# Performance work log

Measured on AMD Instinct MI355X. Metric: run time of the kernel, lower is better.

Reference implementation:

```python
import jax, jax.numpy as jnp
import numpy as np

B, L, R, D = 4, 1024, 4, 1024   # batch, seq, expansion rate, model dim
HEADS, HD, FF = 16, 64, 4096
EPS = 1e-6


def _static_alpha(layer_id):
    a0 = np.zeros((R, 1), np.float32)
    a0[layer_id % R, 0] = 1.0
    return jnp.asarray(np.concatenate([a0, np.eye(R, dtype=np.float32)], axis=1))  # [R, R+1]


def setup_inputs() -> dict:
    key = jax.random.key(0)
    ks = jax.random.split(key, 12)
    w = lambda k, shape, s=0.02: (jax.random.normal(k, shape, jnp.float32) * s)
    return {
        "H": jax.random.normal(ks[0], (B, L, R, D), jnp.float32),
        # attention hyper-connection (layer_id*2 = 0)
        "hc1_norm_w": jnp.ones((D,), jnp.float32),
        "hc1_alpha_fn": w(ks[1], (D, R + 1), 0.01),
        "hc1_beta_fn": w(ks[2], (D,), 0.01),
        "hc1_a_scale": jnp.full((1,), 0.01, jnp.float32),
        "hc1_b_scale": jnp.full((1,), 0.01, jnp.float32),
        "hc1_s_alpha": _static_alpha(0),
        "hc1_s_beta": jnp.ones((R,), jnp.float32),
        # attention
        "attn_norm_w": jnp.ones((D,), jnp.float32),
        "qkv_w": w(ks[3], (3 * D, D)),
        "out_w": w(ks[4], (D, D)),
        # ffn hyper-connection (layer_id*2+1 = 1)
        "hc2_norm_w": jnp.ones((D,), jnp.float32),
        "hc2_alpha_fn": w(ks[5], (D, R + 1), 0.01),
        "hc2_beta_fn": w(ks[6], (D,), 0.01),
        "hc2_a_scale": jnp.full((1,), 0.01, jnp.float32),
        "hc2_b_scale": jnp.full((1,), 0.01, jnp.float32),
        "hc2_s_alpha": _static_alpha(1),
        "hc2_s_beta": jnp.ones((R,), jnp.float32),
        # ffn
        "ffn_norm_w": jnp.ones((D,), jnp.float32),
        "fc1_w": w(ks[7], (FF, D)),
        "fc2_w": w(ks[8], (D, FF)),
    }


def _rms(x, weight):
    norm = jnp.sqrt(jnp.mean(x * x, axis=-1, keepdims=True))
    return weight * x / (norm + EPS)


def _width(Hm, norm_w, alpha_fn, beta_fn, a_scale, b_scale, s_alpha, s_beta):
    nh = _rms(Hm, norm_w)                                      # [B,L,R,D]
    alpha = jnp.tanh(jnp.einsum('blnd,dk->blnk', nh, alpha_fn)) * a_scale + s_alpha  # [B,L,R,R+1]
    beta = jnp.tanh(jnp.einsum('blnd,d->bln', nh, beta_fn)) * b_scale + s_beta       # [B,L,R]
    mix = jnp.einsum('blnk,blnd->blkd', alpha, Hm)             # [B,L,R+1,D]
    return mix, beta


def _depth(mix, out, beta):
    return beta[..., None] * out[:, :, None, :] + mix[..., 1:, :]


def _attention(x, qkv_w, out_w):
    b, l, d = x.shape
    qkv = (x @ qkv_w.T).reshape(b, l, 3, HEADS, HD)
    q, k, v = (jnp.moveaxis(qkv, 2, 0)[i].transpose(0, 2, 1, 3) for i in range(3))  # [B,H,L,HD]
    scores = jnp.einsum('bhqd,bhkd->bhqk', q, k) * (HD ** -0.5)
    causal = jnp.tril(jnp.ones((l, l), bool))
    scores = jnp.where(causal, scores, jnp.float32(-jnp.inf))
    attn = jax.nn.softmax(scores, axis=-1)
    out = jnp.einsum('bhqk,bhkd->bhqd', attn, v).transpose(0, 2, 1, 3).reshape(b, l, d)
    return out @ out_w.T


def reference(H, hc1_norm_w, hc1_alpha_fn, hc1_beta_fn, hc1_a_scale, hc1_b_scale,
              hc1_s_alpha, hc1_s_beta, attn_norm_w, qkv_w, out_w,
              hc2_norm_w, hc2_alpha_fn, hc2_beta_fn, hc2_a_scale, hc2_b_scale,
              hc2_s_alpha, hc2_s_beta, ffn_norm_w, fc1_w, fc2_w):
    # attention block
    mix, beta = _width(H, hc1_norm_w, hc1_alpha_fn, hc1_beta_fn,
                       hc1_a_scale, hc1_b_scale, hc1_s_alpha, hc1_s_beta)
    h = _rms(mix[..., 0, :], attn_norm_w)
    h = _attention(h, qkv_w, out_w)
    H = _depth(mix, h, beta)
    # ffn block
    mix, beta = _width(H, hc2_norm_w, hc2_alpha_fn, hc2_beta_fn,
                       hc2_a_scale, hc2_b_scale, hc2_s_alpha, hc2_s_beta)
    h = _rms(mix[..., 0, :], ffn_norm_w)
    h = (jax.nn.gelu(h @ fc1_w.T, approximate=False)) @ fc2_w.T
    H = _depth(mix, h, beta)
    return H
```

## Files before the change

kernel.cpp:

```cpp
#include <hip/hip_runtime.h>
#include <math.h>

#define BB 4
#define LL 1024
#define RR 4
#define DD 1024
#define NHEADS 16
#define HDIM 64
#define FFD 4096
#define EPSV 1e-6f

typedef short s16x8 __attribute__((ext_vector_type(8)));
typedef float f32x4 __attribute__((ext_vector_type(4)));
typedef unsigned short u16;

__device__ inline unsigned short f2bf(float x) {
  unsigned u = __builtin_bit_cast(unsigned, x);
  unsigned r = (u + 0x7fffu + ((u >> 16) & 1u)) >> 16;
  return (unsigned short)r;
}
__device__ inline float bf2f(u16 x) {
  return __builtin_bit_cast(float, (unsigned)x << 16);
}

__device__ inline float wred_xor(float v) {
#pragma unroll
  for (int off = 1; off < 64; off <<= 1) v += __shfl_xor(v, off);
  return v;
}

__device__ inline void gload_lds16(const u16* g, u16* l) {
  __builtin_amdgcn_global_load_lds(
      (const __attribute__((address_space(1))) unsigned int*)g,
      (__attribute__((address_space(3))) unsigned int*)l, 16, 0, 0);
}

__global__ __launch_bounds__(256) void cvt4_kernel(
    const float* __restrict__ s0, const float* __restrict__ s1,
    const float* __restrict__ s2, const float* __restrict__ s3,
    u16* __restrict__ d0, u16* __restrict__ d1,
    u16* __restrict__ d2, u16* __restrict__ d3) {
  const int n0 = 786432, n1 = 262144, n2 = 1048576, n3 = 1048576;
  const int total = n0 + n1 + n2 + n3;
  for (int i = blockIdx.x * 256 + threadIdx.x; i < total; i += gridDim.x * 256) {
    const float4* src; ushort4* dst; int j;
    if (i < n0)                { src = (const float4*)s0; dst = (ushort4*)d0; j = i; }
    else if (i < n0 + n1)      { src = (const float4*)s1; dst = (ushort4*)d1; j = i - n0; }
    else if (i < n0 + n1 + n2) { src = (const float4*)s2; dst = (ushort4*)d2; j = i - n0 - n1; }
    else                       { src = (const float4*)s3; dst = (ushort4*)d3; j = i - n0 - n1 - n2; }
    float4 v = src[j];
    ushort4 o;
    o.x = f2bf(v.x); o.y = f2bf(v.y); o.z = f2bf(v.z); o.w = f2bf(v.w);
    dst[j] = o;
  }
}

template<int NP>
__global__ __launch_bounds__(256) void width_kernel(
    const float* __restrict__ Hin,
    const u16* __restrict__ mixrest_in,
    const float* __restrict__ beta_in,
    const u16* __restrict__ pp,
    const float* __restrict__ hc_norm_w,
    const float* __restrict__ alpha_fn,
    const float* __restrict__ beta_fn,
    const float* __restrict__ a_scale,
    const float* __restrict__ b_scale,
    const float* __restrict__ s_alpha,
    const float* __restrict__ s_beta,
    const float* __restrict__ post_norm_w,
    u16* __restrict__ mixrest_out,
    float* __restrict__ beta_out,
    u16* __restrict__ x_out)
{
  const size_t MN = (size_t)4096 * 1024;
  const int l = threadIdx.x & 63, w = threadIdx.x >> 6;
  const int bl = blockIdx.x * 4 + w;
  const int d0 = l << 2;

  float4 h[4][4];
  if (NP > 0) {
    float be[4];
#pragma unroll
    for (int n = 0; n < 4; ++n) be[n] = beta_in[bl * 4 + n];
#pragma unroll
    for (int i = 0; i < 4; ++i) {
      const int d = i * 256 + d0;
      float4 s; s.x = 0.f; s.y = 0.f; s.z = 0.f; s.w = 0.f;
#pragma unroll
      for (int p = 0; p < (NP > 0 ? NP : 1); ++p) {
        ushort4 v = *(const ushort4*)&pp[p * MN + (size_t)bl * 1024 + d];
        s.x += bf2f(v.x); s.y += bf2f(v.y); s.z += bf2f(v.z); s.w += bf2f(v.w);
      }
#pragma unroll
      for (int n = 0; n < 4; ++n) {
        ushort4 mr = *(const ushort4*)&mixrest_in[(size_t)bl * 4096 + n * 1024 + d];
        h[n][i].x = be[n] * s.x + bf2f(mr.x);
        h[n][i].y = be[n] * s.y + bf2f(mr.y);
        h[n][i].z = be[n] * s.z + bf2f(mr.z);
        h[n][i].w = be[n] * s.w + bf2f(mr.w);
      }
    }
  } else {
#pragma unroll
    for (int i = 0; i < 4; ++i) {
      const int d = i * 256 + d0;
#pragma unroll
      for (int n = 0; n < 4; ++n)
        h[n][i] = *(const float4*)&Hin[(size_t)bl * 4096 + n * 1024 + d];
    }
  }

  float inv[4];
#pragma unroll
  for (int n = 0; n < 4; ++n) {
    float a = 0.f;
#pragma unroll
    for (int i = 0; i < 4; ++i)
      a += h[n][i].x * h[n][i].x + h[n][i].y * h[n][i].y +
           h[n][i].z * h[n][i].z + h[n][i].w * h[n][i].w;
    a = wred_xor(a);
    inv[n] = 1.f / (sqrtf(a * (1.f / 1024.f)) + EPSV);
  }

  float dots[4][6];
#pragma unroll
  for (int n = 0; n < 4; ++n)
#pragma unroll
    for (int k = 0; k < 6; ++k) dots[n][k] = 0.f;
#pragma unroll
  for (int i = 0; i < 4; ++i) {
    const int d = i * 256 + d0;
    float4 nw = *(const float4*)&hc_norm_w[d];
    float4 bfv4 = *(const float4*)&beta_fn[d];
    float4 A0 = *(const float4*)&alpha_fn[d * 5];
    float4 A1 = *(const float4*)&alpha_fn[d * 5 + 4];
    float4 A2 = *(const float4*)&alpha_fn[d * 5 + 8];
    float4 A3 = *(const float4*)&alpha_fn[d * 5 + 12];
    float4 A4 = *(const float4*)&alpha_fn[d * 5 + 16];
    const float af[4][5] = {
        {A0.x, A0.y, A0.z, A0.w, A1.x},
        {A1.y, A1.z, A1.w, A2.x, A2.y},
        {A2.z, A2.w, A3.x, A3.y, A3.z},
        {A3.w, A4.x, A4.y, A4.z, A4.w}};
    const float nwv[4] = {nw.x, nw.y, nw.z, nw.w};
    const float bfl[4] = {bfv4.x, bfv4.y, bfv4.z, bfv4.w};
#pragma unroll
    for (int j = 0; j < 4; ++j) {
      const float wj = nwv[j];
#pragma unroll
      for (int n = 0; n < 4; ++n) {
        const float hw = (j == 0 ? h[n][i].x : j == 1 ? h[n][i].y : j == 2 ? h[n][i].z : h[n][i].w) * wj;
        dots[n][0] += hw * af[j][0];
        dots[n][1] += hw * af[j][1];
        dots[n][2] += hw * af[j][2];
        dots[n][3] += hw * af[j][3];
        dots[n][4] += hw * af[j][4];
        dots[n][5] += hw * bfl[j];
      }
    }
  }
  const float as = a_scale[0], bs = b_scale[0];
  float alpha[4][5], betav[4];
#pragma unroll
  for (int n = 0; n < 4; ++n) {
#pragma unroll
    for (int k = 0; k < 5; ++k) {
      float r = wred_xor(dots[n][k]);
      alpha[n][k] = tanhf(r * inv[n]) * as + s_alpha[n * 5 + k];
    }
    float rb = wred_xor(dots[n][5]);
    betav[n] = tanhf(rb * inv[n]) * bs + s_beta[n];
  }
  if (l == 0) {
#pragma unroll
    for (int n = 0; n < 4; ++n) beta_out[bl * 4 + n] = betav[n];
  }

  float4 mix0[4];
#pragma unroll
  for (int i = 0; i < 4; ++i) {
    const int d = i * 256 + d0;
#pragma unroll
    for (int k = 0; k < 5; ++k) {
      const float c0 = alpha[0][k], c1 = alpha[1][k], c2 = alpha[2][k], c3 = alpha[3][k];
      float4 mv;
      mv.x = c0 * h[0][i].x + c1 * h[1][i].x + c2 * h[2][i].x + c3 * h[3][i].x;
      mv.y = c0 * h[0][i].y + c1 * h[1][i].y + c2 * h[2][i].y + c3 * h[3][i].y;
      mv.z = c0 * h[0][i].z + c1 * h[1][i].z + c2 * h[2][i].z + c3 * h[3][i].z;
      mv.w = c0 * h[0][i].w + c1 * h[1][i].w + c2 * h[2][i].w + c3 * h[3][i].w;
      if (k == 0) {
        mix0[i] = mv;
      } else {
        ushort4 ov;
        ov.x = f2bf(mv.x); ov.y = f2bf(mv.y); ov.z = f2bf(mv.z); ov.w = f2bf(mv.w);
        *(ushort4*)&mixrest_out[(size_t)bl * 4096 + (size_t)(k - 1) * 1024 + d] = ov;
      }
    }
  }

  float a0s = 0.f;
#pragma unroll
  for (int i = 0; i < 4; ++i)
    a0s += mix0[i].x * mix0[i].x + mix0[i].y * mix0[i].y +
           mix0[i].z * mix0[i].z + mix0[i].w * mix0[i].w;
  a0s = wred_xor(a0s);
  const float iv0 = 1.f / (sqrtf(a0s * (1.f / 1024.f)) + EPSV);
#pragma unroll
  for (int i = 0; i < 4; ++i) {
    const int d = i * 256 + d0;
    float4 pw = *(const float4*)&post_norm_w[d];
    ushort4 ov;
    ov.x = f2bf(pw.x * mix0[i].x * iv0);
    ov.y = f2bf(pw.y * mix0[i].y * iv0);
    ov.z = f2bf(pw.z * mix0[i].z * iv0);
    ov.w = f2bf(pw.w * mix0[i].w * iv0);
    *(ushort4*)&x_out[(size_t)bl * 1024 + d] = ov;
  }
}

template<int EPI, int SPLIT>
__global__ __launch_bounds__(256, 4) void gemm_bt_kernel(
    const u16* __restrict__ A, const u16* __restrict__ W,
    u16* __restrict__ Cb, u16* __restrict__ Vt,
    int M, int N, int K)
{
  __shared__ __align__(16) u16 LDSb[2][2][128 * 32];
  const int tn = N >> 7, tm = M >> 7;
  int bid = blockIdx.x;
  const int nwg = gridDim.x;
  if ((nwg & 7) == 0) bid = (bid & 7) * (nwg >> 3) + (bid >> 3);
  const int ts = tm * tn;
  const int sK = bid / ts;
  const int tb = bid - sK * ts;
  const int bm = tb / tn, bn = tb % tn;
  const int Kc = K / SPLIT;
  const int kbeg = sK * Kc;

  const int t = threadIdx.x, l = t & 63, w = t >> 6;
  const int wr = w >> 1, wc = w & 1;
  const int m0 = bm << 7, n0 = bn << 7;
  const int ssc = (((l & 3) ^ ((l >> 3) & 3)) << 3);
  const int srA = m0 + (w << 5) + (l >> 2);
  const int srB = n0 + (w << 5) + (l >> 2);
  const int ldso = (w << 10);
  const int fr = l & 15, g4 = l >> 4;
  const int fc8 = ((g4 ^ ((l >> 1) & 3)) << 3);

  f32x4 acc[4][4];
#pragma unroll
  for (int i = 0; i < 4; ++i)
#pragma unroll
    for (int j = 0; j < 4; ++j)
#pragma unroll
      for (int e = 0; e < 4; ++e) acc[i][j][e] = 0.f;

  const u16* pa0 = A + (size_t)srA * K + kbeg + ssc;
  const u16* pa1 = A + (size_t)(srA + 16) * K + kbeg + ssc;
  const u16* pb0 = W + (size_t)srB * K + kbeg + ssc;
  const u16* pb1 = W + (size_t)(srB + 16) * K + kbeg + ssc;

#define STAGE(buf, koff)                                   \
  do {                                                     \
    gload_lds16(pa0 + (koff), &LDSb[buf][0][ldso]);        \
    gload_lds16(pa1 + (koff), &LDSb[buf][0][ldso + 512]);  \
    gload_lds16(pb0 + (koff), &LDSb[buf][1][ldso]);        \
    gload_lds16(pb1 + (koff), &LDSb[buf][1][ldso + 512]);  \
  } while (0)

  const int nt = Kc >> 5;
  STAGE(0, 0);
  int cur = 0;
  for (int kt = 0; kt < nt; ++kt) {
    if (kt + 1 < nt) {
      STAGE(cur ^ 1, (kt + 1) << 5);
      asm volatile("s_waitcnt vmcnt(4)" ::: "memory");
    } else {
      asm volatile("s_waitcnt vmcnt(0)" ::: "memory");
    }
    __builtin_amdgcn_s_barrier();
    __builtin_amdgcn_sched_barrier(0);
    s16x8 af[4], bfr[4];
#pragma unroll
    for (int m = 0; m < 4; ++m)
      af[m] = *(const s16x8*)(&LDSb[cur][0][(wr * 64 + m * 16 + fr) * 32 + fc8]);
#pragma unroll
    for (int n = 0; n < 4; ++n)
      bfr[n] = *(const s16x8*)(&LDSb[cur][1][(wc * 64 + n * 16 + fr) * 32 + fc8]);
#pragma unroll
    for (int m = 0; m < 4; ++m)
#pragma unroll
      for (int n = 0; n < 4; ++n)
        acc[m][n] = __builtin_amdgcn_mfma_f32_16x16x32_bf16(af[m], bfr[n], acc[m][n], 0, 0, 0);
    asm volatile("s_waitcnt lgkmcnt(0)" ::: "memory");
    __builtin_amdgcn_sched_barrier(0);
    __builtin_amdgcn_s_barrier();
    cur ^= 1;
  }
#undef STAGE

  if (EPI == 2 && n0 >= 2048) {
    const int rbv = m0 + wr * 64 + (g4 << 2);
    const int cbv = n0 + wc * 64 + fr;
#pragma unroll
    for (int m = 0; m < 4; ++m)
#pragma unroll
      for (int n = 0; n < 4; ++n) {
        int cc = cbv + n * 16 - 2048;
        int hh = cc >> 6, dd = cc & 63;
        int r0 = rbv + m * 16;
        ushort4 ov;
        ov.x = f2bf(acc[m][n][0]); ov.y = f2bf(acc[m][n][1]);
        ov.z = f2bf(acc[m][n][2]); ov.w = f2bf(acc[m][n][3]);
        *(ushort4*)&Vt[((size_t)((r0 >> 10) * 16 + hh) * 64 + dd) * 1024 + (r0 & 1023)] = ov;
      }
    return;
  }

  float* scr = (float*)LDSb;
  const int strideN = (EPI == 2) ? 2048 : N;
  u16* Cout = (SPLIT > 1) ? (Cb + (size_t)sK * M * N) : Cb;
#pragma unroll
  for (int r = 0; r < 2; ++r) {
    __syncthreads();
    if (wr == r) {
#pragma unroll
      for (int m = 0; m < 4; ++m)
#pragma unroll
        for (int n = 0; n < 4; ++n)
#pragma unroll
          for (int j = 0; j < 4; ++j) {
            int lr = m * 16 + (g4 << 2) + j;
            int col = wc * 64 + n * 16 + fr;
            scr[lr * 128 + (col ^ ((((lr >> 2) & 7)) << 3))] = acc[m][n][j];
          }
    }
    __syncthreads();
#pragma unroll
    for (int it = 0; it < 4; ++it) {
      int lr = it * 16 + (t >> 4);
      int key8 = ((lr >> 2) & 7) << 3;
      int lc = (t & 15) << 3;
      int cb0 = (lc ^ key8);
      f32x4 v0 = *(const f32x4*)&scr[lr * 128 + cb0];
      f32x4 v1 = *(const f32x4*)&scr[lr * 128 + cb0 + 4];
      float vv[8] = {v0[0], v0[1], v0[2], v0[3], v1[0], v1[1], v1[2], v1[3]};
      s16x8 ov;
#pragma unroll
      for (int c = 0; c < 8; ++c) {
        float v = vv[c];
        if (EPI == 1) v = 0.5f * v * (1.f + erff(v * 0.70710678118f));
        ov[c] = (short)f2bf(v);
      }
      size_t gr = (size_t)(m0 + r * 64 + lr);
      *(s16x8*)&Cout[gr * strideN + n0 + lc] = ov;
    }
  }
}

template<int EPI, int SPLIT>
__global__ __launch_bounds__(512, 1) void gemm256_kernel(
    const u16* __restrict__ A, const u16* __restrict__ W,
    u16* __restrict__ Cb,
    int M, int N, int K)
{
  __shared__ __align__(16) u16 As[2][256 * 64];
  __shared__ __align__(16) u16 Bs[2][256 * 64];
  const int tn = N >> 8, tm = M >> 8;
  int bid = blockIdx.x;
  const int nwg = gridDim.x;
  bid = (bid & 7) * (nwg >> 3) + (bid >> 3);
  const int ts = tm * tn;
  const int sK = bid / ts;
  const int tb = bid - sK * ts;
  const int bm = tb / tn, bn = tb % tn;
  const int Kc = K / SPLIT;
  const int kbeg = sK * Kc;

  const int t = threadIdx.x, l = t & 63, w = t >> 6;
  const int wr = w >> 2, wc = w & 3;
  const int m0g = bm << 8, n0g = bn << 8;
  const int fr = l & 15, g4 = l >> 4;

  const int srow = t >> 3;
  const int gsc8 = (((t & 7) ^ (srow & 7)) << 3);
  const u16* pA = A + (size_t)(m0g + srow) * K + kbeg + gsc8;
  const u16* pB = W + (size_t)(n0g + srow) * K + kbeg + gsc8;

#define STG_A(rb, buf, ko) gload_lds16(pA + (size_t)(rb) * K + (ko), &As[buf][(rb) * 64 + (t << 3)])
#define STG_B(rb, buf, ko) gload_lds16(pB + (size_t)(rb) * K + (ko), &Bs[buf][(rb) * 64 + (t << 3)])
#define LDA(dst, mh, kk)                                                                   \
  {                                                                                        \
    _Pragma("unroll") for (int j = 0; j < 4; ++j)                                          \
        dst[j] = *(const s16x8*)(&As[c][(wr * 128 + ((mh)*4 + j) * 16 + fr) * 64 +         \
                                        ((((kk)*4 + g4) ^ (fr & 7)) << 3)]);               \
  }
#define LDB(dst, kk)                                                                       \
  {                                                                                        \
    _Pragma("unroll") for (int n = 0; n < 4; ++n)                                          \
        dst[n] = *(const s16x8*)(&Bs[c][(wc * 64 + n * 16 + fr) * 64 +                     \
                                        ((((kk)*4 + g4) ^ (fr & 7)) << 3)]);               \
  }
#define MM(mh, BF)                                                                         \
  _Pragma("unroll") for (int j = 0; j < 4; ++j)                                            \
      _Pragma("unroll") for (int n = 0; n < 4; ++n)                                        \
          acc[(mh)*4 + j][n] =                                                             \
              __builtin_amdgcn_mfma_f32_16x16x32_bf16(af[j], BF[n], acc[(mh)*4 + j][n], 0, 0, 0);
#define LGKM0                                            \
  asm volatile("s_waitcnt lgkmcnt(0)" ::: "memory");     \
  __builtin_amdgcn_sched_barrier(0)
#define BAR                                              \
  __builtin_amdgcn_s_barrier();                          \
  __builtin_amdgcn_sched_barrier(0)

  f32x4 acc[8][4];
#pragma unroll
  for (int i = 0; i < 8; ++i)
#pragma unroll
    for (int j = 0; j < 4; ++j)
#pragma unroll
      for (int e = 0; e < 4; ++e) acc[i][j][e] = 0.f;

  const int nt = Kc >> 6;
  STG_B(0, 0, 0); STG_B(64, 0, 0);
  STG_B(128, 0, 0); STG_B(192, 0, 0);
  STG_A(0, 0, 0); STG_A(128, 0, 0);
  STG_A(64, 0, 0); STG_A(192, 0, 0);

  int c = 0;
  for (int kt = 0; kt < nt; ++kt) {
    const bool st = (kt + 1 < nt);
    const int ko = (kt + 1) << 6;
    const int nb = c ^ 1;
    s16x8 af[4], bf0[4], bf1[4];
    asm volatile("s_waitcnt vmcnt(2)" ::: "memory");
    BAR;
    if (st) { STG_B(0, nb, ko); STG_B(64, nb, ko); }
    LDA(af, 0, 0); LDB(bf0, 0);
    LGKM0;
    __builtin_amdgcn_s_setprio(1); MM(0, bf0); __builtin_amdgcn_s_setprio(0);
    BAR;
    if (st) { STG_B(128, nb, ko); STG_B(192, nb, ko); }
    LDA(af, 0, 1); LDB(bf1, 1);
    LGKM0;
    __builtin_amdgcn_s_setprio(1); MM(0, bf1); __builtin_amdgcn_s_setprio(0);
    if (st) asm volatile("s_waitcnt vmcnt(4)" ::: "memory");
    else    asm volatile("s_waitcnt vmcnt(0)" ::: "memory");
    BAR;
    if (st) { STG_A(0, nb, ko); STG_A(128, nb, ko); }
    LDA(af, 1, 0);
    LGKM0;
    __builtin_amdgcn_s_setprio(1); MM(1, bf0); __builtin_amdgcn_s_setprio(0);
    BAR;
    if (st) { STG_A(64, nb, ko); STG_A(192, nb, ko); }
    LDA(af, 1, 1);
    LGKM0;
    __builtin_amdgcn_s_setprio(1); MM(1, bf1); __builtin_amdgcn_s_setprio(0);
    c = nb;
  }
#undef STG_A
#undef STG_B
#undef LDA
#undef LDB
#undef MM
#undef LGKM0
#undef BAR

  float* scr = (float*)As;
  u16* Cout = (SPLIT > 1) ? (Cb + (size_t)sK * M * N) : Cb;
#pragma unroll
  for (int rb = 0; rb < 4; ++rb) {
    __syncthreads();
    if (wr == (rb >> 1)) {
      const int mlo = (rb & 1) * 4;
#pragma unroll
      for (int mm = 0; mm < 4; ++mm)
#pragma unroll
        for (int n = 0; n < 4; ++n)
#pragma unroll
          for (int j = 0; j < 4; ++j) {
            int lr = mm * 16 + (g4 << 2) + j;
            int col = wc * 64 + n * 16 + fr;
            scr[lr * 256 + (col ^ (((lr >> 2) & 7) << 3))] = acc[mlo + mm][n][j];
          }
    }
    __syncthreads();
#pragma unroll
    for (int it = 0; it < 4; ++it) {
      int lr = it * 16 + (t >> 5);
      int key8 = ((lr >> 2) & 7) << 3;
      int lc = (t & 31) << 3;
      int cb0 = lc ^ key8;
      f32x4 v0 = *(const f32x4*)&scr[lr * 256 + cb0];
      f32x4 v1 = *(const f32x4*)&scr[lr * 256 + cb0 + 4];
      float vv[8] = {v0[0], v0[1], v0[2], v0[3], v1[0], v1[1], v1[2], v1[3]};
      s16x8 ov;
#pragma unroll
      for (int cc = 0; cc < 8; ++cc) {
        float v = vv[cc];
        if (EPI == 1) v = 0.5f * v * (1.f + erff(v * 0.70710678118f));
        ov[cc] = (short)f2bf(v);
      }
      size_t gr = (size_t)(m0g + rb * 64 + lr);
      *(s16x8*)&Cout[gr * N + n0g + lc] = ov;
    }
  }
}

__global__ __launch_bounds__(256) void attn_mfma_kernel(
    const u16* __restrict__ qk, const u16* __restrict__ Vt, u16* __restrict__ out)
{
  const int id = blockIdx.x;
  const int hb = id & 63, qt0 = id >> 6;
  const int b = hb >> 4, h = hb & 15;
  const int qt = (h & 1) ? (15 - qt0) : qt0;
  const int t = threadIdx.x, l = t & 63, w = t >> 6;
  const int q0 = qt << 6;
  __shared__ __align__(16) u16 Ks[2][64 * 64];
  __shared__ __align__(16) u16 Vs[2][64 * 64];
  __shared__ __align__(16) u16 Ps[4][16 * 64];

  const int fr = l & 15;
  const int fg = (l >> 4) << 3;
  const int fswz = (fr & 7) << 3;

  const int qrow = q0 + w * 16 + fr;
  const size_t qbase = (size_t)(b * 1024 + qrow) * 2048 + h * 64 + fg;
  const s16x8 aq0 = *(const s16x8*)(qk + qbase);
  const s16x8 aq1 = *(const s16x8*)(qk + qbase + 32);

  f32x4 acc_o[4];
#pragma unroll
  for (int i = 0; i < 4; ++i)
#pragma unroll
    for (int e = 0; e < 4; ++e) acc_o[i][e] = 0.f;
  float m_i[4] = {-INFINITY, -INFINITY, -INFINITY, -INFINITY};
  float l_i[4] = {0.f, 0.f, 0.f, 0.f};

  const int sr = (w << 3) + (l >> 3);
  const int scs = (((l & 7) ^ ((l >> 3) & 7)) << 3);
  const u16* ksrc = qk + (size_t)(b * 1024 + sr) * 2048 + 1024 + h * 64 + scs;
  const u16* vsrc = Vt + ((size_t)((b * 16 + h) * 64 + sr)) * 1024 + scs;
  const int ldst = (w << 9);

#define ASTAGE(buf, kb_)                                                     \
  do {                                                                       \
    gload_lds16(ksrc + (size_t)(kb_) * 2048, &Ks[buf][ldst]);                \
    gload_lds16(ksrc + (size_t)((kb_) + 32) * 2048, &Ks[buf][2048 + ldst]);  \
    gload_lds16(vsrc + (kb_), &Vs[buf][ldst]);                               \
    gload_lds16(vsrc + (kb_) + 32 * 1024, &Vs[buf][2048 + ldst]);            \
  } while (0)

  const int qrow_c = q0 + w * 16 + ((l >> 4) << 2);
  u16* Psw = &Ps[w][0];
  const int nkt = qt + 1;

  ASTAGE(0, 0);
  int cur = 0;
  for (int kt = 0; kt < nkt; ++kt) {
    const int kb = kt << 6;
    if (kt + 1 < nkt) {
      ASTAGE(cur ^ 1, (kt + 1) << 6);
      asm volatile("s_waitcnt vmcnt(4)" ::: "memory");
    } else {
      asm volatile("s_waitcnt vmcnt(0)" ::: "memory");
    }
    __builtin_amdgcn_s_barrier();
    __builtin_amdgcn_sched_barrier(0);

    f32x4 s[4];
#pragma unroll
    for (int n = 0; n < 4; ++n) {
#pragma unroll
      for (int e = 0; e < 4; ++e) s[n][e] = 0.f;
      s16x8 bk0 = *(const s16x8*)(&Ks[cur][(n * 16 + fr) * 64 + (fg ^ fswz)]);
      s16x8 bk1 = *(const s16x8*)(&Ks[cur][(n * 16 + fr) * 64 + ((32 + fg) ^ fswz)]);
      s[n] = __builtin_amdgcn_mfma_f32_16x16x32_bf16(aq0, bk0, s[n], 0, 0, 0);
      s[n] = __builtin_amdgcn_mfma_f32_16x16x32_bf16(aq1, bk1, s[n], 0, 0, 0);
    }
#pragma unroll
    for (int n = 0; n < 4; ++n)
#pragma unroll
      for (int e = 0; e < 4; ++e) s[n][e] *= 0.125f;
    if (kt == nkt - 1 && kb == q0) {
#pragma unroll
      for (int n = 0; n < 4; ++n) {
        int kc = kb + n * 16 + fr;
#pragma unroll
        for (int r = 0; r < 4; ++r)
          if (kc > qrow_c + r) s[n][r] = -INFINITY;
      }
    }

    float rm[4], fac[4];
#pragma unroll
    for (int r = 0; r < 4; ++r)
      rm[r] = fmaxf(fmaxf(s[0][r], s[1][r]), fmaxf(s[2][r], s[3][r]));
#pragma unroll
    for (int off = 1; off < 16; off <<= 1)
#pragma unroll
      for (int r = 0; r < 4; ++r) rm[r] = fmaxf(rm[r], __shfl_xor(rm[r], off));
#pragma unroll
    for (int r = 0; r < 4; ++r) {
      float mn = fmaxf(m_i[r], rm[r]);
      fac[r] = __expf(m_i[r] - mn);
      m_i[r] = mn;
    }
    float rs[4] = {0.f, 0.f, 0.f, 0.f};
    float pb[4][4];
#pragma unroll
    for (int n = 0; n < 4; ++n)
#pragma unroll
      for (int r = 0; r < 4; ++r) {
        float pv = __expf(s[n][r] - m_i[r]);
        pb[n][r] = pv;
        rs[r] += pv;
      }
#pragma unroll
    for (int off = 1; off < 16; off <<= 1)
#pragma unroll
      for (int r = 0; r < 4; ++r) rs[r] += __shfl_xor(rs[r], off);
#pragma unroll
    for (int r = 0; r < 4; ++r) l_i[r] = l_i[r] * fac[r] + rs[r];
#pragma unroll
    for (int dt = 0; dt < 4; ++dt)
#pragma unroll
      for (int r = 0; r < 4; ++r) acc_o[dt][r] *= fac[r];

#pragma unroll
    for (int n = 0; n < 4; ++n)
#pragma unroll
      for (int r = 0; r < 4; ++r) {
        int prow = ((l >> 4) << 2) + r;
        Psw[prow * 64 + ((n * 16 + fr) ^ ((prow & 7) << 3))] = f2bf(pb[n][r]);
      }
    asm volatile("s_waitcnt lgkmcnt(0)" ::: "memory");
    __builtin_amdgcn_sched_barrier(0);

    s16x8 pa0 = *(const s16x8*)(Psw + fr * 64 + (fg ^ fswz));
    s16x8 pa1 = *(const s16x8*)(Psw + fr * 64 + ((32 + fg) ^ fswz));
#pragma unroll
    for (int dt = 0; dt < 4; ++dt) {
      s16x8 bv0 = *(const s16x8*)(&Vs[cur][(dt * 16 + fr) * 64 + (fg ^ fswz)]);
      s16x8 bv1 = *(const s16x8*)(&Vs[cur][(dt * 16 + fr) * 64 + ((32 + fg) ^ fswz)]);
      acc_o[dt] = __builtin_amdgcn_mfma_f32_16x16x32_bf16(pa0, bv0, acc_o[dt], 0, 0, 0);
      acc_o[dt] = __builtin_amdgcn_mfma_f32_16x16x32_bf16(pa1, bv1, acc_o[dt], 0, 0, 0);
    }
    asm volatile("s_waitcnt lgkmcnt(0)" ::: "memory");
    __builtin_amdgcn_sched_barrier(0);
    __builtin_amdgcn_s_barrier();
    cur ^= 1;
  }
#undef ASTAGE

  float invl[4];
#pragma unroll
  for (int r = 0; r < 4; ++r) invl[r] = 1.f / l_i[r];
#pragma unroll
  for (int dt = 0; dt < 4; ++dt)
#pragma unroll
    for (int r = 0; r < 4; ++r) {
      size_t idx = (size_t)(b * 1024 + qrow_c + r) * 1024 + h * 64 + dt * 16 + fr;
      out[idx] = f2bf(acc_o[dt][r] * invl[r]);
    }
}

template<int NPART>
__global__ __launch_bounds__(256) void depth2_kernel(
    const u16* __restrict__ parts, const u16* __restrict__ mixrest,
    const float* __restrict__ beta, float* __restrict__ Hout)
{
  const size_t MN = (size_t)4096 * 1024;
  const size_t stride = (size_t)gridDim.x * 256;
  const size_t n8 = (size_t)BB * LL * RR * DD / 8;
  for (size_t i = (size_t)blockIdx.x * 256 + threadIdx.x; i < n8; i += stride) {
    size_t e = i * 8;
    int d = (int)(e & 1023);
    int n = (int)((e >> 10) & 3);
    size_t bl = e >> 12;
    float be = beta[bl * 4 + n];
    float f[8];
#pragma unroll
    for (int j = 0; j < 8; ++j) f[j] = 0.f;
#pragma unroll
    for (int p = 0; p < NPART; ++p) {
      s16x8 v = *(const s16x8*)&parts[p * MN + bl * 1024 + d];
#pragma unroll
      for (int j = 0; j < 8; ++j) f[j] += bf2f((u16)v[j]);
    }
    s16x8 m = *(const s16x8*)&mixrest[e];
    float4 o0, o1;
    o0.x = be * f[0] + bf2f((u16)m[0]); o0.y = be * f[1] + bf2f((u16)m[1]);
    o0.z = be * f[2] + bf2f((u16)m[2]); o0.w = be * f[3] + bf2f((u16)m[3]);
    o1.x = be * f[4] + bf2f((u16)m[4]); o1.y = be * f[5] + bf2f((u16)m[5]);
    o1.z = be * f[6] + bf2f((u16)m[6]); o1.w = be * f[7] + bf2f((u16)m[7]);
    *(float4*)&Hout[e] = o0;
    *(float4*)&Hout[e + 4] = o1;
  }
}

extern "C" void kernel_launch(void* const* d_in, const int* in_sizes, int n_in,
                              void* d_out, int out_size, void* d_ws, size_t ws_size,
                              hipStream_t stream) {
  const float* H       = (const float*)d_in[0];
  const float* hc1_nw  = (const float*)d_in[1];
  const float* hc1_afn = (const float*)d_in[2];
  const float* hc1_bfn = (const float*)d_in[3];
  const float* hc1_as  = (const float*)d_in[4];
  const float* hc1_bs  = (const float*)d_in[5];
  const float* hc1_sa  = (const float*)d_in[6];
  const float* hc1_sb  = (const float*)d_in[7];
  const float* attn_nw = (const float*)d_in[8];
  const float* qkv_w   = (const float*)d_in[9];
  const float* out_w   = (const float*)d_in[10];
  const float* hc2_nw  = (const float*)d_in[11];
  const float* hc2_afn = (const float*)d_in[12];
  const float* hc2_bfn = (const float*)d_in[13];
  const float* hc2_as  = (const float*)d_in[14];
  const float* hc2_bs  = (const float*)d_in[15];
  const float* hc2_sa  = (const float*)d_in[16];
  const float* hc2_sb  = (const float*)d_in[17];
  const float* ffn_nw  = (const float*)d_in[18];
  const float* fc1_w   = (const float*)d_in[19];
  const float* fc2_w   = (const float*)d_in[20];
  float* Hout = (float*)d_out;

  char* wsp = (char*)d_ws;
  size_t off = 0;
  auto carve = [&](size_t bytes) {
    void* p = wsp + off;
    off = (off + bytes + 255) & ~(size_t)255;
    return p;
  };
  const size_t MN = (size_t)4096 * 1024;
  u16* wq_bf   = (u16*)carve((size_t)3072 * 1024 * 2);
  u16* wo_bf   = (u16*)carve((size_t)1024 * 1024 * 2);
  u16* w1_bf   = (u16*)carve((size_t)4096 * 1024 * 2);
  u16* w2_bf   = (u16*)carve((size_t)4096 * 1024 * 2);
  u16* xbf     = (u16*)carve((size_t)4096 * 1024 * 2);
  u16* mixrest = (u16*)carve((size_t)4096 * 4096 * 2);
  float* beta1 = (float*)carve((size_t)16384 * 4);
  float* beta2 = (float*)carve((size_t)16384 * 4);
  char* uregion = (char*)carve((size_t)32 * 1024 * 1024);
  u16* qk_bf   = (u16*)uregion;
  u16* Vt      = (u16*)(uregion + (size_t)16 * 1024 * 1024);
  u16* g1_bf   = (u16*)uregion;
  u16* attn_bf = (u16*)carve((size_t)4096 * 1024 * 2);
  u16* pp      = (u16*)carve((size_t)4 * MN * 2);

  cvt4_kernel<<<2048, 256, 0, stream>>>(qkv_w, out_w, fc1_w, fc2_w, wq_bf, wo_bf, w1_bf, w2_bf);
  width_kernel<0><<<1024, 256, 0, stream>>>(H, nullptr, nullptr, nullptr,
      hc1_nw, hc1_afn, hc1_bfn, hc1_as, hc1_bs, hc1_sa, hc1_sb, attn_nw,
      mixrest, beta1, xbf);
  gemm_bt_kernel<2, 1><<<768, 256, 0, stream>>>(xbf, wq_bf, qk_bf, Vt, 4096, 3072, 1024);
  attn_mfma_kernel<<<1024, 256, 0, stream>>>(qk_bf, Vt, attn_bf);
  gemm_bt_kernel<0, 4><<<1024, 256, 0, stream>>>(attn_bf, wo_bf, pp, nullptr, 4096, 1024, 1024);
  width_kernel<4><<<1024, 256, 0, stream>>>(nullptr, mixrest, beta1, pp,
      hc2_nw, hc2_afn, hc2_bfn, hc2_as, hc2_bs, hc2_sa, hc2_sb, ffn_nw,
      mixrest, beta2, xbf);
  gemm256_kernel<1, 1><<<256, 512, 0, stream>>>(xbf, w1_bf, g1_bf, 4096, 4096, 1024);
  gemm256_kernel<0, 4><<<256, 512, 0, stream>>>(g1_bf, w2_bf, pp, 4096, 1024, 4096);
  depth2_kernel<4><<<4096, 256, 0, stream>>>(pp, mixrest, beta2, Hout);
}
```

Baseline: 328.4 us.

## Restructure gemm256 prefetch to issue a whole tile two steps ahead; use gemm_bt for fc2

The 256x256 GEMM main loop previously interleaved staged global-to-LDS loads of the next tile between MFMA phases. It now prefetches two full tiles in the prologue and, at the end of each iteration, issues all eight loads for tile kt+2 into the buffer just consumed, waiting on vmcnt so the next tile is ready. Extra barriers are added around the LDS fragment reads. Separately, the fc2 GEMM switches from gemm256_kernel to gemm_bt_kernel with split-K 4 and 1024 blocks of 256 threads, aiming for better occupancy and load balance. The added barriers and the coarser prefetch granularity may reduce overlap between loads and MFMA work.

```diff
diff --git a/kernel.cpp b/kernel.cpp
--- a/kernel.cpp
+++ b/kernel.cpp
@@ -389,6 +389,14 @@
 
 #define STG_A(rb, buf, ko) gload_lds16(pA + (size_t)(rb) * K + (ko), &As[buf][(rb) * 64 + (t << 3)])
 #define STG_B(rb, buf, ko) gload_lds16(pB + (size_t)(rb) * K + (ko), &Bs[buf][(rb) * 64 + (t << 3)])
+#define STAGE8(buf, kt_)                                         \
+  do {                                                           \
+    const int ko_ = (kt_) << 6;                                  \
+    STG_B(0, buf, ko_);  STG_B(64, buf, ko_);                    \
+    STG_B(128, buf, ko_); STG_B(192, buf, ko_);                  \
+    STG_A(0, buf, ko_);  STG_A(64, buf, ko_);                    \
+    STG_A(128, buf, ko_); STG_A(192, buf, ko_);                  \
+  } while (0)
 #define LDA(dst, mh, kk)                                                                   \
   {                                                                                        \
     _Pragma("unroll") for (int j = 0; j < 4; ++j)                                          \
@@ -422,44 +430,44 @@
       for (int e = 0; e < 4; ++e) acc[i][j][e] = 0.f;
 
   const int nt = Kc >> 6;
-  STG_B(0, 0, 0); STG_B(64, 0, 0);
-  STG_B(128, 0, 0); STG_B(192, 0, 0);
-  STG_A(0, 0, 0); STG_A(128, 0, 0);
-  STG_A(64, 0, 0); STG_A(192, 0, 0);
+  STAGE8(0, 0);
+  STAGE8(1, 1);
+  asm volatile("s_waitcnt vmcnt(8)" ::: "memory");
+  __builtin_amdgcn_s_barrier();
+  __builtin_amdgcn_sched_barrier(0);
 
   int c = 0;
   for (int kt = 0; kt < nt; ++kt) {
-    const bool st = (kt + 1 < nt);
-    const int ko = (kt + 1) << 6;
-    const int nb = c ^ 1;
     s16x8 af[4], bf0[4], bf1[4];
-    asm volatile("s_waitcnt vmcnt(2)" ::: "memory");
-    BAR;
-    if (st) { STG_B(0, nb, ko); STG_B(64, nb, ko); }
     LDA(af, 0, 0); LDB(bf0, 0);
-    LGKM0;
+    BAR; LGKM0;
     __builtin_amdgcn_s_setprio(1); MM(0, bf0); __builtin_amdgcn_s_setprio(0);
     BAR;
-    if (st) { STG_B(128, nb, ko); STG_B(192, nb, ko); }
     LDA(af, 0, 1); LDB(bf1, 1);
-    LGKM0;
+    BAR; LGKM0;
     __builtin_amdgcn_s_setprio(1); MM(0, bf1); __builtin_amdgcn_s_setprio(0);
-    if (st) asm volatile("s_waitcnt vmcnt(4)" ::: "memory");
-    else    asm volatile("s_waitcnt vmcnt(0)" ::: "memory");
     BAR;
-    if (st) { STG_A(0, nb, ko); STG_A(128, nb, ko); }
     LDA(af, 1, 0);
-    LGKM0;
+    BAR; LGKM0;
     __builtin_amdgcn_s_setprio(1); MM(1, bf0); __builtin_amdgcn_s_setprio(0);
     BAR;
-    if (st) { STG_A(64, nb, ko); STG_A(192, nb, ko); }
     LDA(af, 1, 1);
-    LGKM0;
+    BAR; LGKM0;
     __builtin_amdgcn_s_setprio(1); MM(1, bf1); __builtin_amdgcn_s_setprio(0);
-    c = nb;
+    BAR;
+    if (kt + 2 < nt) {
+      STAGE8(c, kt + 2);
+      asm volatile("s_waitcnt vmcnt(8)" ::: "memory");
+      BAR;
+    } else if (kt + 1 < nt) {
+      asm volatile("s_waitcnt vmcnt(0)" ::: "memory");
+      BAR;
+    }
+    c ^= 1;
   }
 #undef STG_A
 #undef STG_B
+#undef STAGE8
 #undef LDA
 #undef LDB
 #undef MM
@@ -759,6 +767,6 @@
       hc2_nw, hc2_afn, hc2_bfn, hc2_as, hc2_bs, hc2_sa, hc2_sb, ffn_nw,
       mixrest, beta2, xbf);
   gemm256_kernel<1, 1><<<256, 512, 0, stream>>>(xbf, w1_bf, g1_bf, 4096, 4096, 1024);
-  gemm256_kernel<0, 4><<<256, 512, 0, stream>>>(g1_bf, w2_bf, pp, 4096, 1024, 4096);
+  gemm_bt_kernel<0, 4><<<1024, 256, 0, stream>>>(g1_bf, w2_bf, pp, nullptr, 4096, 1024, 4096);
   depth2_kernel<4><<<4096, 256, 0, stream>>>(pp, mixrest, beta2, Hout);
 }
```

Measured after the change: 320.1 us. 1.03x faster.
